# Kernel optimization log

Measured on AMD Instinct MI355X. Metric: run time of the kernel, lower is better.

The kernel has to match this reference:

```python
import math
import jax, jax.numpy as jnp
import numpy as np

B, NQ, NK, DIM, H, HD = 2, 1024, 2048, 1024, 16, 64


def setup_inputs() -> dict:
    key = jax.random.key(0)
    ks = jax.random.split(key, 12)
    s = 1.0 / math.sqrt(DIM)
    return {
        "q": jax.random.normal(ks[0], (B, NQ, DIM), jnp.float32),
        "k": jax.random.normal(ks[1], (B, NK, DIM), jnp.float32),
        "v": jax.random.normal(ks[2], (B, NK, DIM), jnp.float32),
        "distances": jax.random.uniform(ks[3], (B, NQ, NK), jnp.float32),
        "attn_mask": jax.random.bernoulli(ks[4], 0.5, (B, NQ, NK)),
        "key_padding_mask_q": jax.random.bernoulli(ks[5], 0.5, (B, NQ)),
        "key_padding_mask_k": jax.random.bernoulli(ks[6], 0.5, (B, NK)),
        "Wq": jax.random.normal(ks[7], (H * HD, DIM), jnp.float32) * s,
        "Wk": jax.random.normal(ks[8], (H * HD, DIM), jnp.float32) * s,
        "Wv": jax.random.normal(ks[9], (H * HD, DIM), jnp.float32) * s,
        "Wo": jax.random.normal(ks[10], (DIM, H * HD), jnp.float32) * s,
        "gate_alpha": jnp.float32(0.1),
    }


def reference(q, k, v, distances, attn_mask, key_padding_mask_q,
              key_padding_mask_k, Wq, Wk, Wv, Wo, gate_alpha):
    bsz, q_len, _ = q.shape
    k_len = k.shape[1]
    neg = jnp.finfo(q.dtype).min

    # projections -> (B, H, N, HD)
    qp = (q @ Wq.T).reshape(bsz, q_len, H, HD).transpose(0, 2, 1, 3)
    kp = (k @ Wk.T).reshape(bsz, k_len, H, HD).transpose(0, 2, 1, 3)
    vp = (v @ Wv.T).reshape(bsz, k_len, H, HD).transpose(0, 2, 1, 3)

    scores = jnp.einsum('bhqd,bhkd->bhqk', qp, kp) / math.sqrt(HD)
    scores = jnp.where(attn_mask[:, None, :, :], scores, neg)
    scores = jnp.where(key_padding_mask_k[:, None, None, :], scores, neg)

    attn = jax.nn.softmax(scores, axis=-1)  # (B,H,NQ,NK)

    # distance gating: mask, batch-mean normalize, exponential gate
    d = distances * attn_mask.astype(distances.dtype)
    d = d * key_padding_mask_k[:, None, :].astype(d.dtype)
    mean = d.sum(axis=(-1, -2)) / (q_len * k_len + 1e-6)
    mean = jnp.maximum(mean, 1e-6)[:, None, None]
    d = d / mean
    alpha = jax.nn.softplus(gate_alpha)
    gate = jnp.exp(-alpha * d)[:, None, :, :]  # (B,1,NQ,NK)

    w = attn * gate
    w = w / (w.sum(axis=-1, keepdims=True) + 1e-6)

    out = jnp.einsum('bhqk,bhkd->bhqd', w, vp)
    out = out.transpose(0, 2, 1, 3).reshape(bsz, q_len, H * HD)
    out = out * key_padding_mask_q[:, :, None].astype(out.dtype)
    return out @ Wo.T
```

## Files before the change

kernel.cpp:

```cpp
#include <hip/hip_runtime.h>
#include <hip/hip_bf16.h>
#include <cfloat>

#define B_   2
#define NQ_  1024
#define NK_  2048
#define H_   16
#define HD_  64
#define VPAD 2176
#define GPAD 2112
#define NSPLIT 2

typedef float  floatx4 __attribute__((ext_vector_type(4)));
typedef __bf16 bf16x8  __attribute__((ext_vector_type(8)));
typedef __bf16 bf16x4  __attribute__((ext_vector_type(4)));

static __device__ __forceinline__ floatx4 mfma16(bf16x8 a, bf16x8 b, floatx4 c) {
    return __builtin_amdgcn_mfma_f32_16x16x32_bf16(a, b, c, 0, 0, 0);
}

static __device__ __forceinline__ void gl_lds(const __bf16* g, __bf16* lbase,
                                              int lane) {
#if __has_builtin(__builtin_amdgcn_global_load_lds)
    __builtin_amdgcn_global_load_lds(
        (const __attribute__((address_space(1))) void*)g,
        (__attribute__((address_space(3))) void*)lbase, 16, 0, 0);
#else
    *(bf16x8*)(lbase + lane * 8) = *(const bf16x8*)g;
#endif
}

struct CvtArgs {
    const float* src[7];
    __bf16*      dst[7];
};

__global__ __launch_bounds__(256) void cvt_mean_kernel(
    CvtArgs a, const float* __restrict__ dist, const int* __restrict__ amask,
    const int* __restrict__ kpmk, float* __restrict__ msum,
    __bf16* __restrict__ dmask)
{
    if (blockIdx.x >= 7168) {
        const int mb = blockIdx.x - 7168;
        const int b  = mb >> 7;
        const float* d  = dist  + (size_t)b * NQ_ * NK_;
        const int*   am = amask + (size_t)b * NQ_ * NK_;
        const int*   km = kpmk  + b * NK_;
        __bf16*      dm = dmask + (size_t)b * NQ_ * GPAD;
        const int total = NQ_ * NK_ / 4;
        float s = 0.f;
        for (int i = (mb & 127) * 256 + threadIdx.x; i < total; i += 128 * 256) {
            const int idx = i * 4;
            const int kk  = idx & (NK_ - 1);
            const int q   = i >> 9;
            float4 dv = *(const float4*)(d + idx);
            int4   mv = *(const int4*)(am + idx);
            int4   kv = *(const int4*)(km + kk);
            bf16x4 o;
            if (mv.x && kv.x) { s += dv.x; o[0] = (__bf16)dv.x; } else o[0] = (__bf16)3e38f;
            if (mv.y && kv.y) { s += dv.y; o[1] = (__bf16)dv.y; } else o[1] = (__bf16)3e38f;
            if (mv.z && kv.z) { s += dv.z; o[2] = (__bf16)dv.z; } else o[2] = (__bf16)3e38f;
            if (mv.w && kv.w) { s += dv.w; o[3] = (__bf16)dv.w; } else o[3] = (__bf16)3e38f;
            *(bf16x4*)&dm[(size_t)q * GPAD + kk] = o;
        }
        #pragma unroll
        for (int off = 32; off >= 1; off >>= 1) s += __shfl_down(s, off);
        __shared__ float wsum[4];
        if ((threadIdx.x & 63) == 0) wsum[threadIdx.x >> 6] = s;
        __syncthreads();
        if (threadIdx.x == 0)
            atomicAdd(&msum[b], wsum[0] + wsum[1] + wsum[2] + wsum[3]);
        return;
    }
    size_t r = (size_t)blockIdx.x * 256 + threadIdx.x;
    int s;
    if (r < 262144)                  { s = 0; }
    else if ((r -= 262144) < 524288) { s = 1; }
    else if ((r -= 524288) < 524288) { s = 2; }
    else { r -= 524288; s = 3 + (int)(r >> 17); r &= 131071; }
    const float* sp = a.src[s] + r * 8;
    float4 f0 = *(const float4*)sp;
    float4 f1 = *(const float4*)(sp + 4);
    bf16x8 o;
    o[0] = (__bf16)f0.x; o[1] = (__bf16)f0.y; o[2] = (__bf16)f0.z; o[3] = (__bf16)f0.w;
    o[4] = (__bf16)f1.x; o[5] = (__bf16)f1.y; o[6] = (__bf16)f1.z; o[7] = (__bf16)f1.w;
    *(bf16x8*)(a.dst[s] + r * 8) = o;
}

template <typename EPI>
static __device__ __forceinline__ void gemm128_core(
    const __bf16* __restrict__ A, const __bf16* __restrict__ Bw,
    int m0, int n0, __bf16* As, __bf16* Bs, EPI epi)
{
    const int t    = threadIdx.x;
    const int w    = t >> 6, lane = t & 63;
    const int lrow = lane & 15, quad = lane >> 4;
    const int lr   = lane >> 2, lc = lane & 3;

    floatx4 acc[4][4];
    #pragma unroll
    for (int mi = 0; mi < 4; mi++)
        #pragma unroll
        for (int ni = 0; ni < 4; ni++) acc[mi][ni] = floatx4{0.f, 0.f, 0.f, 0.f};

    const __bf16* ga = A  + (size_t)(m0 + w * 32 + lr) * 1024 + lc * 8;
    const __bf16* gb = Bw + (size_t)(n0 + w * 32 + lr) * 1024 + lc * 8;

    for (int k0 = 0; k0 < 1024; k0 += 64) {
        __syncthreads();
        #pragma unroll
        for (int h = 0; h < 2; h++) {
            gl_lds(ga + k0 + h * 32,             &As[h * 4096 + (w * 32) * 32],      lane);
            gl_lds(ga + k0 + h * 32 + 16 * 1024, &As[h * 4096 + (w * 32 + 16) * 32], lane);
            gl_lds(gb + k0 + h * 32,             &Bs[h * 4096 + (w * 32) * 32],      lane);
            gl_lds(gb + k0 + h * 32 + 16 * 1024, &Bs[h * 4096 + (w * 32 + 16) * 32], lane);
        }
        __syncthreads();

        #pragma unroll
        for (int h = 0; h < 2; h++) {
            bf16x8 af[4], bfr[4];
            #pragma unroll
            for (int mi = 0; mi < 4; mi++)
                af[mi] = *(const bf16x8*)
                    &As[h * 4096 + ((w & 1) * 64 + mi * 16 + lrow) * 32 + quad * 8];
            #pragma unroll
            for (int ni = 0; ni < 4; ni++)
                bfr[ni] = *(const bf16x8*)
                    &Bs[h * 4096 + ((w >> 1) * 64 + ni * 16 + lrow) * 32 + quad * 8];
            #pragma unroll
            for (int mi = 0; mi < 4; mi++)
                #pragma unroll
                for (int ni = 0; ni < 4; ni++)
                    acc[mi][ni] = mfma16(af[mi], bfr[ni], acc[mi][ni]);
        }
    }

    #pragma unroll
    for (int mi = 0; mi < 4; mi++)
        #pragma unroll
        for (int ni = 0; ni < 4; ni++)
            #pragma unroll
            for (int r = 0; r < 4; r++) {
                const int m = m0 + (w & 1) * 64 + mi * 16 + quad * 4 + r;
                const int n = n0 + (w >> 1) * 64 + ni * 16 + lrow;
                epi(m, n, acc[mi][ni][r]);
            }
}

template <typename EPI>
static __device__ __forceinline__ void gemm64_core(
    const __bf16* __restrict__ A, const __bf16* __restrict__ Bw,
    int m0, int n0, EPI epi)
{
    __shared__ alignas(16) __bf16 As[2][64 * 32];
    __shared__ alignas(16) __bf16 Bs[2][128 * 32];
    const int t    = threadIdx.x;
    const int w    = t >> 6, lane = t & 63;
    const int lrow = lane & 15, quad = lane >> 4;
    const int lr   = lane >> 2, lc = lane & 3;

    floatx4 acc[4][2];
    #pragma unroll
    for (int mi = 0; mi < 4; mi++)
        #pragma unroll
        for (int ni = 0; ni < 2; ni++) acc[mi][ni] = floatx4{0.f, 0.f, 0.f, 0.f};

    const __bf16* ga = A  + (size_t)(m0 + w * 16 + lr) * 1024 + lc * 8;
    const __bf16* gb = Bw + (size_t)(n0 + w * 32 + lr) * 1024 + lc * 8;

    for (int k0 = 0; k0 < 1024; k0 += 64) {
        __syncthreads();
        #pragma unroll
        for (int h = 0; h < 2; h++) {
            gl_lds(ga + k0 + h * 32,             &As[h][(w * 16) * 32],      lane);
            gl_lds(gb + k0 + h * 32,             &Bs[h][(w * 32) * 32],      lane);
            gl_lds(gb + k0 + h * 32 + 16 * 1024, &Bs[h][(w * 32 + 16) * 32], lane);
        }
        __syncthreads();

        #pragma unroll
        for (int h = 0; h < 2; h++) {
            bf16x8 af[4], bfr[2];
            #pragma unroll
            for (int mi = 0; mi < 4; mi++)
                af[mi] = *(const bf16x8*)
                    &As[h][(mi * 16 + lrow) * 32 + quad * 8];
            #pragma unroll
            for (int ni = 0; ni < 2; ni++)
                bfr[ni] = *(const bf16x8*)
                    &Bs[h][(w * 32 + ni * 16 + lrow) * 32 + quad * 8];
            #pragma unroll
            for (int mi = 0; mi < 4; mi++)
                #pragma unroll
                for (int ni = 0; ni < 2; ni++)
                    acc[mi][ni] = mfma16(af[mi], bfr[ni], acc[mi][ni]);
        }
    }

    #pragma unroll
    for (int mi = 0; mi < 4; mi++)
        #pragma unroll
        for (int ni = 0; ni < 2; ni++)
            #pragma unroll
            for (int r = 0; r < 4; r++) {
                const int m = m0 + mi * 16 + quad * 4 + r;
                const int n = n0 + w * 32 + ni * 16 + lrow;
                epi(m, n, acc[mi][ni][r]);
            }
}

__global__ __launch_bounds__(256) void proj_kernel(
    const __bf16* __restrict__ qb, const __bf16* __restrict__ kb,
    const __bf16* __restrict__ vb, const __bf16* __restrict__ wqb,
    const __bf16* __restrict__ wkb, const __bf16* __restrict__ wvb,
    __bf16* __restrict__ qp, __bf16* __restrict__ kp,
    __bf16* __restrict__ vpT)
{
    __shared__ alignas(16) __bf16 As[2 * 128 * 32];
    __shared__ alignas(16) __bf16 Bs[2 * 128 * 32];
    const int z = blockIdx.z;
    if (z == 0) {
        if ((int)blockIdx.x >= 16) return;
        gemm128_core(qb, wqb, blockIdx.x * 128, blockIdx.y * 128, As, Bs,
                     [&](int m, int n, float v) {
            const int b = m >> 10, q = m & 1023;
            const int h = n >> 6,  d = n & 63;
            qp[(((size_t)(b * 16 + h) * NQ_ + q) << 6) + d] = (__bf16)v;
        });
    } else if (z == 1) {
        gemm128_core(kb, wkb, blockIdx.x * 128, blockIdx.y * 128, As, Bs,
                     [&](int m, int n, float v) {
            const int b = m >> 11, key = m & 2047;
            const int h = n >> 6,  d = n & 63;
            kp[(((size_t)(b * 16 + h) * NK_ + key) << 6) + d] = (__bf16)v;
        });
    } else {
        gemm128_core(wvb, vb, blockIdx.y * 128, blockIdx.x * 128, As, Bs,
                     [&](int m, int n, float v) {
            const int h = m >> 6,  d = m & 63;
            const int b = n >> 11, key = n & 2047;
            vpT[((size_t)(b * 16 + h) * HD_ + d) * VPAD + key] = (__bf16)v;
        });
    }
}

__global__ __launch_bounds__(256) void oproj_kernel(
    const __bf16* __restrict__ A, const __bf16* __restrict__ W,
    float* __restrict__ Cout)
{
    const int m0 = blockIdx.x * 64, n0 = blockIdx.y * 128;
    gemm64_core(A, W, m0, n0, [&](int m, int n, float v) {
        Cout[(size_t)m * 1024 + n] = v;
    });
}

__global__ __launch_bounds__(256, 2) void attn_kernel(
    const __bf16* __restrict__ qp, const __bf16* __restrict__ kp,
    const __bf16* __restrict__ vpT, const __bf16* __restrict__ dmask,
    const float* __restrict__ msum, const float* __restrict__ galpha,
    float* __restrict__ Opart, float* __restrict__ Gpart)
{
    __shared__ __bf16 Ks[64 * 72];
    __shared__ __bf16 Vt[2][64 * 72];
    __shared__ __bf16 Ps[4][2][32 * 72];
    const int t    = threadIdx.x;
    const int w    = t >> 6, lane = t & 63;
    const int lrow = lane & 15, quad = lane >> 4;
    const int qt   = blockIdx.x;
    const int bh   = blockIdx.y;
    const int sp   = blockIdx.z;
    const int b    = bh >> 4;
    const int q0   = qt * 128 + w * 32;
    const int k0   = sp * (NK_ / NSPLIT);
    const int NT   = (NK_ / NSPLIT) / 64;

    const float mean  = fmaxf(msum[b] / ((float)(NQ_ * NK_) + 1e-6f), 1e-6f);
    const float alpha = log1pf(__expf(galpha[0]));
    const float cg    = -alpha / mean;

    bf16x8 qf[2][2];
    #pragma unroll
    for (int qg = 0; qg < 2; qg++) {
        const __bf16* qb = qp + ((size_t)bh * NQ_ + q0 + qg * 16 + lrow) * HD_ +
                           quad * 8;
        qf[qg][0] = *(const bf16x8*)qb;
        qf[qg][1] = *(const bf16x8*)(qb + 32);
    }

    const int srow0 = t >> 3,        sc0 = t & 7;
    const int srow1 = 32 + (t >> 3), sc1 = t & 7;
    const int so0 = srow0 * 72 + sc0 * 8;
    const int so1 = srow1 * 72 + sc1 * 8;
    const __bf16* Kg = kp  + (size_t)bh * NK_ * HD_;
    const __bf16* Vg = vpT + (size_t)bh * HD_ * VPAD;

    const __bf16* grow[2];
    #pragma unroll
    for (int qg = 0; qg < 2; qg++)
        grow[qg] = dmask + ((size_t)b * NQ_ + q0 + qg * 16 + lrow) * GPAD;

    float G[2] = {0.f, 0.f};
    floatx4 O[2][4];
    #pragma unroll
    for (int qg = 0; qg < 2; qg++)
        #pragma unroll
        for (int nb = 0; nb < 4; nb++) O[qg][nb] = floatx4{0.f, 0.f, 0.f, 0.f};

    bf16x8 kr0, kr1, vr0, vr1;
    bf16x4 gr[2][4];
    auto loadt = [&](int kb) {
        kr0 = *(const bf16x8*)(Kg + (size_t)(kb + srow0) * HD_ + sc0 * 8);
        kr1 = *(const bf16x8*)(Kg + (size_t)(kb + srow1) * HD_ + sc1 * 8);
        vr0 = *(const bf16x8*)(Vg + (size_t)srow0 * VPAD + kb + sc0 * 8);
        vr1 = *(const bf16x8*)(Vg + (size_t)srow1 * VPAD + kb + sc1 * 8);
        #pragma unroll
        for (int qg = 0; qg < 2; qg++)
            #pragma unroll
            for (int c = 0; c < 4; c++)
                gr[qg][c] = *(const bf16x4*)(grow[qg] + kb + c * 16 + quad * 4);
    };
    loadt(k0);

    for (int ib = 0; ib < NT; ib++) {
        const int kb  = k0 + ib * 64;
        const int cur = ib & 1;

        __syncthreads();
        *(bf16x8*)&Ks[so0]      = kr0;
        *(bf16x8*)&Ks[so1]      = kr1;
        *(bf16x8*)&Vt[cur][so0] = vr0;
        *(bf16x8*)&Vt[cur][so1] = vr1;
        __syncthreads();

        bf16x4 gcur[2][4];
        #pragma unroll
        for (int qg = 0; qg < 2; qg++)
            #pragma unroll
            for (int c = 0; c < 4; c++) gcur[qg][c] = gr[qg][c];
        if (ib + 1 < NT) loadt(kb + 64);

        bf16x8 kf0[4], kf1[4];
        #pragma unroll
        for (int c = 0; c < 4; c++) {
            kf0[c] = *(const bf16x8*)&Ks[(c * 16 + lrow) * 72 + quad * 8];
            kf1[c] = *(const bf16x8*)&Ks[(c * 16 + lrow) * 72 + 32 + quad * 8];
        }
        floatx4 s4[2][4];
        #pragma unroll
        for (int qg = 0; qg < 2; qg++)
            #pragma unroll
            for (int c = 0; c < 4; c++) {
                floatx4 a = floatx4{0.f, 0.f, 0.f, 0.f};
                a = mfma16(kf0[c], qf[qg][0], a);
                a = mfma16(kf1[c], qf[qg][1], a);
                s4[qg][c] = a;
            }

        if (ib > 0) {
            const int prv = cur ^ 1;
            bf16x8 pf[2][2];
            #pragma unroll
            for (int qg = 0; qg < 2; qg++)
                #pragma unroll
                for (int tt = 0; tt < 2; tt++)
                    pf[qg][tt] = *(const bf16x8*)
                        &Ps[w][prv][(qg * 16 + lrow) * 72 + tt * 32 + quad * 8];
            #pragma unroll
            for (int tt = 0; tt < 2; tt++)
                #pragma unroll
                for (int nb = 0; nb < 4; nb++) {
                    bf16x8 vf = *(const bf16x8*)
                        &Vt[prv][(nb * 16 + lrow) * 72 + tt * 32 + quad * 8];
                    #pragma unroll
                    for (int qg = 0; qg < 2; qg++)
                        O[qg][nb] = mfma16(pf[qg][tt], vf, O[qg][nb]);
                }
        }

        #pragma unroll
        for (int qg = 0; qg < 2; qg++) {
            #pragma unroll
            for (int c = 0; c < 4; c++) {
                const float e0 = __expf(fmaf(s4[qg][c][0], 0.125f, cg * (float)gcur[qg][c][0]));
                const float e1 = __expf(fmaf(s4[qg][c][1], 0.125f, cg * (float)gcur[qg][c][1]));
                const float e2 = __expf(fmaf(s4[qg][c][2], 0.125f, cg * (float)gcur[qg][c][2]));
                const float e3 = __expf(fmaf(s4[qg][c][3], 0.125f, cg * (float)gcur[qg][c][3]));
                G[qg] += (e0 + e1) + (e2 + e3);
                bf16x4 pk;
                pk[0] = (__bf16)e0; pk[1] = (__bf16)e1;
                pk[2] = (__bf16)e2; pk[3] = (__bf16)e3;
                *(bf16x4*)&Ps[w][cur][(qg * 16 + lrow) * 72 + c * 16 + quad * 4] = pk;
            }
        }
    }

    {
        const int prv = (NT - 1) & 1;
        bf16x8 pf[2][2];
        #pragma unroll
        for (int qg = 0; qg < 2; qg++)
            #pragma unroll
            for (int tt = 0; tt < 2; tt++)
                pf[qg][tt] = *(const bf16x8*)
                    &Ps[w][prv][(qg * 16 + lrow) * 72 + tt * 32 + quad * 8];
        #pragma unroll
        for (int tt = 0; tt < 2; tt++)
            #pragma unroll
            for (int nb = 0; nb < 4; nb++) {
                bf16x8 vf = *(const bf16x8*)
                    &Vt[prv][(nb * 16 + lrow) * 72 + tt * 32 + quad * 8];
                #pragma unroll
                for (int qg = 0; qg < 2; qg++)
                    O[qg][nb] = mfma16(pf[qg][tt], vf, O[qg][nb]);
            }
    }

    #pragma unroll
    for (int qg = 0; qg < 2; qg++) {
        G[qg] += __shfl_xor(G[qg], 16);
        G[qg] += __shfl_xor(G[qg], 32);
    }
    float* Ob = Opart + ((size_t)(sp * 32 + bh) * NQ_ + q0) * HD_;
    #pragma unroll
    for (int qg = 0; qg < 2; qg++)
        #pragma unroll
        for (int nb = 0; nb < 4; nb++)
            #pragma unroll
            for (int r = 0; r < 4; r++)
                Ob[(size_t)(qg * 16 + quad * 4 + r) * HD_ + nb * 16 + lrow] =
                    O[qg][nb][r];
    if (quad == 0) {
        #pragma unroll
        for (int qg = 0; qg < 2; qg++)
            Gpart[(size_t)(sp * 32 + bh) * NQ_ + q0 + qg * 16 + lrow] = G[qg];
    }
}

__global__ __launch_bounds__(256) void combine_kernel(
    const float* __restrict__ Opart, const float* __restrict__ Gpart,
    const int* __restrict__ kpmq, __bf16* __restrict__ attnout)
{
    const int t  = blockIdx.x * 256 + threadIdx.x;
    const int d4 = (t & 15) * 4;
    const int q  = (t >> 4) & 1023;
    const int bh = t >> 14;
    const int b  = bh >> 4, h = bh & 15;
    float4 o = float4{0.f, 0.f, 0.f, 0.f};
    float  g = 0.f;
    #pragma unroll
    for (int j = 0; j < NSPLIT; j++) {
        float4 oj = *(const float4*)
            (Opart + ((size_t)(j * 32 + bh) * NQ_ + q) * HD_ + d4);
        o.x += oj.x; o.y += oj.y; o.z += oj.z; o.w += oj.w;
        g += Gpart[(size_t)(j * 32 + bh) * NQ_ + q];
    }
    const float f = kpmq[b * NQ_ + q] ? 1.f / (g + 1e-30f) : 0.f;
    bf16x4 r;
    r[0] = (__bf16)(o.x * f);
    r[1] = (__bf16)(o.y * f);
    r[2] = (__bf16)(o.z * f);
    r[3] = (__bf16)(o.w * f);
    *(bf16x4*)&attnout[((size_t)b * NQ_ + q) * 1024 + h * HD_ + d4] = r;
}

extern "C" void kernel_launch(void* const* d_in, const int* in_sizes, int n_in,
                              void* d_out, int out_size, void* d_ws,
                              size_t ws_size, hipStream_t stream)
{
    const float* q      = (const float*)d_in[0];
    const float* k      = (const float*)d_in[1];
    const float* v      = (const float*)d_in[2];
    const float* dist   = (const float*)d_in[3];
    const int*   amask  = (const int*)d_in[4];
    const int*   kpmq   = (const int*)d_in[5];
    const int*   kpmk   = (const int*)d_in[6];
    const float* Wq     = (const float*)d_in[7];
    const float* Wk     = (const float*)d_in[8];
    const float* Wv     = (const float*)d_in[9];
    const float* Wo     = (const float*)d_in[10];
    const float* galpha = (const float*)d_in[11];

    char* p = (char*)d_ws;
    float*  msum = (float*)p;                 p += 256;
    __bf16* qb   = (__bf16*)p;                p += (size_t)2097152 * 2;
    __bf16* kb   = (__bf16*)p;                p += (size_t)4194304 * 2;
    __bf16* vb   = (__bf16*)p;                p += (size_t)4194304 * 2;
    __bf16* wqb  = (__bf16*)p;                p += (size_t)1048576 * 2;
    __bf16* wkb  = (__bf16*)p;                p += (size_t)1048576 * 2;
    __bf16* wvb  = (__bf16*)p;                p += (size_t)1048576 * 2;
    __bf16* wob  = (__bf16*)p;                p += (size_t)1048576 * 2;
    __bf16* qp   = (__bf16*)p;                p += (size_t)2097152 * 2;
    __bf16* kpb  = (__bf16*)p;                p += (size_t)4194304 * 2;
    __bf16* vpT  = (__bf16*)p;                p += (size_t)32 * 64 * VPAD * 2;
    __bf16* dmask = (__bf16*)p;               p += (size_t)2048 * GPAD * 2;
    __bf16* attnout = (__bf16*)p;             p += (size_t)2097152 * 2;
    float*  Opart   = (float*)p;              p += (size_t)NSPLIT * 2097152 * 4;
    float*  Gpart   = (float*)p;              p += (size_t)NSPLIT * 32768 * 4;

    CvtArgs ca;
    ca.src[0] = q;  ca.src[1] = k;  ca.src[2] = v;
    ca.src[3] = Wq; ca.src[4] = Wk; ca.src[5] = Wv; ca.src[6] = Wo;
    ca.dst[0] = qb;  ca.dst[1] = kb;  ca.dst[2] = vb;
    ca.dst[3] = wqb; ca.dst[4] = wkb; ca.dst[5] = wvb; ca.dst[6] = wob;

    hipMemsetAsync(msum, 0, 256, stream);
    cvt_mean_kernel<<<7424, 256, 0, stream>>>(ca, dist, amask, kpmk, msum,
                                              dmask);
    proj_kernel<<<dim3(32, 8, 3), 256, 0, stream>>>(qb, kb, vb, wqb, wkb, wvb,
                                                    qp, kpb, vpT);
    attn_kernel<<<dim3(8, 32, NSPLIT), 256, 0, stream>>>(qp, kpb, vpT, dmask,
                                                         msum, galpha,
                                                         Opart, Gpart);
    combine_kernel<<<2048, 256, 0, stream>>>(Opart, Gpart, kpmq, attnout);
    oproj_kernel<<<dim3(32, 8), 256, 0, stream>>>(attnout, wob, (float*)d_out);
}
```

Baseline: 258.6 us.

## Drop key split in attention, fuse normalization epilogue, and coarsen conversion blocks

The attention kernel no longer splits the key range across two blocks. Each block now handles 64 queries (16 per wave) over the full key length and writes the normalized, query-masked bf16 output directly, which removes the separate combine kernel and the fp32 partial buffers. The conversion/mean kernel also processes four elements per thread with fewer blocks. In exchange each wave reuses every K/V tile across half as many queries, and the loop runs twice as many serial iterations per block.

```diff
diff --git a/kernel.cpp b/kernel.cpp
--- a/kernel.cpp
+++ b/kernel.cpp
@@ -9,7 +9,6 @@
 #define HD_  64
 #define VPAD 2176
 #define GPAD 2112
-#define NSPLIT 2
 
 typedef float  floatx4 __attribute__((ext_vector_type(4)));
 typedef __bf16 bf16x8  __attribute__((ext_vector_type(8)));
@@ -40,16 +39,18 @@
     const int* __restrict__ kpmk, float* __restrict__ msum,
     __bf16* __restrict__ dmask)
 {
-    if (blockIdx.x >= 7168) {
-        const int mb = blockIdx.x - 7168;
-        const int b  = mb >> 7;
+    if (blockIdx.x >= 1792) {
+        const int mb = blockIdx.x - 1792;
+        const int b  = mb >> 9;
         const float* d  = dist  + (size_t)b * NQ_ * NK_;
         const int*   am = amask + (size_t)b * NQ_ * NK_;
         const int*   km = kpmk  + b * NK_;
         __bf16*      dm = dmask + (size_t)b * NQ_ * GPAD;
-        const int total = NQ_ * NK_ / 4;
+        const int base = (mb & 511) * 256 + threadIdx.x;
         float s = 0.f;
-        for (int i = (mb & 127) * 256 + threadIdx.x; i < total; i += 128 * 256) {
+        #pragma unroll
+        for (int j = 0; j < 4; j++) {
+            const int i   = base + j * 131072;
             const int idx = i * 4;
             const int kk  = idx & (NK_ - 1);
             const int q   = i >> 9;
@@ -72,19 +73,22 @@
             atomicAdd(&msum[b], wsum[0] + wsum[1] + wsum[2] + wsum[3]);
         return;
     }
-    size_t r = (size_t)blockIdx.x * 256 + threadIdx.x;
-    int s;
-    if (r < 262144)                  { s = 0; }
-    else if ((r -= 262144) < 524288) { s = 1; }
-    else if ((r -= 524288) < 524288) { s = 2; }
-    else { r -= 524288; s = 3 + (int)(r >> 17); r &= 131071; }
-    const float* sp = a.src[s] + r * 8;
-    float4 f0 = *(const float4*)sp;
-    float4 f1 = *(const float4*)(sp + 4);
-    bf16x8 o;
-    o[0] = (__bf16)f0.x; o[1] = (__bf16)f0.y; o[2] = (__bf16)f0.z; o[3] = (__bf16)f0.w;
-    o[4] = (__bf16)f1.x; o[5] = (__bf16)f1.y; o[6] = (__bf16)f1.z; o[7] = (__bf16)f1.w;
-    *(bf16x8*)(a.dst[s] + r * 8) = o;
+    #pragma unroll
+    for (int j = 0; j < 4; j++) {
+        size_t r = (size_t)blockIdx.x * 1024 + j * 256 + threadIdx.x;
+        int s;
+        if (r < 262144)                  { s = 0; }
+        else if ((r -= 262144) < 524288) { s = 1; }
+        else if ((r -= 524288) < 524288) { s = 2; }
+        else { r -= 524288; s = 3 + (int)(r >> 17); r &= 131071; }
+        const float* sp = a.src[s] + r * 8;
+        float4 f0 = *(const float4*)sp;
+        float4 f1 = *(const float4*)(sp + 4);
+        bf16x8 o;
+        o[0] = (__bf16)f0.x; o[1] = (__bf16)f0.y; o[2] = (__bf16)f0.z; o[3] = (__bf16)f0.w;
+        o[4] = (__bf16)f1.x; o[5] = (__bf16)f1.y; o[6] = (__bf16)f1.z; o[7] = (__bf16)f1.w;
+        *(bf16x8*)(a.dst[s] + r * 8) = o;
+    }
 }
 
 template <typename EPI>
@@ -259,34 +263,27 @@
     const __bf16* __restrict__ qp, const __bf16* __restrict__ kp,
     const __bf16* __restrict__ vpT, const __bf16* __restrict__ dmask,
     const float* __restrict__ msum, const float* __restrict__ galpha,
-    float* __restrict__ Opart, float* __restrict__ Gpart)
+    const int* __restrict__ kpmq, __bf16* __restrict__ attnout)
 {
     __shared__ __bf16 Ks[64 * 72];
     __shared__ __bf16 Vt[2][64 * 72];
-    __shared__ __bf16 Ps[4][2][32 * 72];
+    __shared__ __bf16 Ps[4][2][16 * 72];
     const int t    = threadIdx.x;
     const int w    = t >> 6, lane = t & 63;
     const int lrow = lane & 15, quad = lane >> 4;
     const int qt   = blockIdx.x;
     const int bh   = blockIdx.y;
-    const int sp   = blockIdx.z;
-    const int b    = bh >> 4;
-    const int q0   = qt * 128 + w * 32;
-    const int k0   = sp * (NK_ / NSPLIT);
-    const int NT   = (NK_ / NSPLIT) / 64;
+    const int b    = bh >> 4, h = bh & 15;
+    const int q0   = qt * 64 + w * 16;
+    const int NT   = NK_ / 64;
 
     const float mean  = fmaxf(msum[b] / ((float)(NQ_ * NK_) + 1e-6f), 1e-6f);
     const float alpha = log1pf(__expf(galpha[0]));
     const float cg    = -alpha / mean;
 
-    bf16x8 qf[2][2];
-    #pragma unroll
-    for (int qg = 0; qg < 2; qg++) {
-        const __bf16* qb = qp + ((size_t)bh * NQ_ + q0 + qg * 16 + lrow) * HD_ +
-                           quad * 8;
-        qf[qg][0] = *(const bf16x8*)qb;
-        qf[qg][1] = *(const bf16x8*)(qb + 32);
-    }
+    const __bf16* qb = qp + ((size_t)bh * NQ_ + q0 + lrow) * HD_ + quad * 8;
+    const bf16x8 qf0 = *(const bf16x8*)qb;
+    const bf16x8 qf1 = *(const bf16x8*)(qb + 32);
 
     const int srow0 = t >> 3,        sc0 = t & 7;
     const int srow1 = 32 + (t >> 3), sc1 = t & 7;
@@ -294,36 +291,28 @@
     const int so1 = srow1 * 72 + sc1 * 8;
     const __bf16* Kg = kp  + (size_t)bh * NK_ * HD_;
     const __bf16* Vg = vpT + (size_t)bh * HD_ * VPAD;
-
-    const __bf16* grow[2];
-    #pragma unroll
-    for (int qg = 0; qg < 2; qg++)
-        grow[qg] = dmask + ((size_t)b * NQ_ + q0 + qg * 16 + lrow) * GPAD;
-
-    float G[2] = {0.f, 0.f};
-    floatx4 O[2][4];
-    #pragma unroll
-    for (int qg = 0; qg < 2; qg++)
-        #pragma unroll
-        for (int nb = 0; nb < 4; nb++) O[qg][nb] = floatx4{0.f, 0.f, 0.f, 0.f};
+    const __bf16* grow = dmask + ((size_t)b * NQ_ + q0 + lrow) * GPAD;
+
+    float G = 0.f;
+    floatx4 O[4];
+    #pragma unroll
+    for (int nb = 0; nb < 4; nb++) O[nb] = floatx4{0.f, 0.f, 0.f, 0.f};
 
     bf16x8 kr0, kr1, vr0, vr1;
-    bf16x4 gr[2][4];
+    bf16x4 gr[4];
     auto loadt = [&](int kb) {
         kr0 = *(const bf16x8*)(Kg + (size_t)(kb + srow0) * HD_ + sc0 * 8);
         kr1 = *(const bf16x8*)(Kg + (size_t)(kb + srow1) * HD_ + sc1 * 8);
         vr0 = *(const bf16x8*)(Vg + (size_t)srow0 * VPAD + kb + sc0 * 8);
         vr1 = *(const bf16x8*)(Vg + (size_t)srow1 * VPAD + kb + sc1 * 8);
         #pragma unroll
-        for (int qg = 0; qg < 2; qg++)
-            #pragma unroll
-            for (int c = 0; c < 4; c++)
-                gr[qg][c] = *(const bf16x4*)(grow[qg] + kb + c * 16 + quad * 4);
+        for (int c = 0; c < 4; c++)
+            gr[c] = *(const bf16x4*)(grow + kb + c * 16 + quad * 4);
     };
-    loadt(k0);
+    loadt(0);
 
     for (int ib = 0; ib < NT; ib++) {
-        const int kb  = k0 + ib * 64;
+        const int kb  = ib * 64;
         const int cur = ib & 1;
 
         __syncthreads();
@@ -333,135 +322,78 @@
         *(bf16x8*)&Vt[cur][so1] = vr1;
         __syncthreads();
 
-        bf16x4 gcur[2][4];
-        #pragma unroll
-        for (int qg = 0; qg < 2; qg++)
-            #pragma unroll
-            for (int c = 0; c < 4; c++) gcur[qg][c] = gr[qg][c];
+        bf16x4 gcur[4];
+        #pragma unroll
+        for (int c = 0; c < 4; c++) gcur[c] = gr[c];
         if (ib + 1 < NT) loadt(kb + 64);
 
-        bf16x8 kf0[4], kf1[4];
+        floatx4 s4[4];
         #pragma unroll
         for (int c = 0; c < 4; c++) {
-            kf0[c] = *(const bf16x8*)&Ks[(c * 16 + lrow) * 72 + quad * 8];
-            kf1[c] = *(const bf16x8*)&Ks[(c * 16 + lrow) * 72 + 32 + quad * 8];
-        }
-        floatx4 s4[2][4];
-        #pragma unroll
-        for (int qg = 0; qg < 2; qg++)
-            #pragma unroll
-            for (int c = 0; c < 4; c++) {
-                floatx4 a = floatx4{0.f, 0.f, 0.f, 0.f};
-                a = mfma16(kf0[c], qf[qg][0], a);
-                a = mfma16(kf1[c], qf[qg][1], a);
-                s4[qg][c] = a;
-            }
+            bf16x8 kf0 = *(const bf16x8*)&Ks[(c * 16 + lrow) * 72 + quad * 8];
+            bf16x8 kf1 = *(const bf16x8*)&Ks[(c * 16 + lrow) * 72 + 32 + quad * 8];
+            floatx4 a = floatx4{0.f, 0.f, 0.f, 0.f};
+            a = mfma16(kf0, qf0, a);
+            a = mfma16(kf1, qf1, a);
+            s4[c] = a;
+        }
 
         if (ib > 0) {
             const int prv = cur ^ 1;
-            bf16x8 pf[2][2];
-            #pragma unroll
-            for (int qg = 0; qg < 2; qg++)
-                #pragma unroll
-                for (int tt = 0; tt < 2; tt++)
-                    pf[qg][tt] = *(const bf16x8*)
-                        &Ps[w][prv][(qg * 16 + lrow) * 72 + tt * 32 + quad * 8];
-            #pragma unroll
-            for (int tt = 0; tt < 2; tt++)
-                #pragma unroll
-                for (int nb = 0; nb < 4; nb++) {
-                    bf16x8 vf = *(const bf16x8*)
-                        &Vt[prv][(nb * 16 + lrow) * 72 + tt * 32 + quad * 8];
-                    #pragma unroll
-                    for (int qg = 0; qg < 2; qg++)
-                        O[qg][nb] = mfma16(pf[qg][tt], vf, O[qg][nb]);
-                }
-        }
-
-        #pragma unroll
-        for (int qg = 0; qg < 2; qg++) {
-            #pragma unroll
-            for (int c = 0; c < 4; c++) {
-                const float e0 = __expf(fmaf(s4[qg][c][0], 0.125f, cg * (float)gcur[qg][c][0]));
-                const float e1 = __expf(fmaf(s4[qg][c][1], 0.125f, cg * (float)gcur[qg][c][1]));
-                const float e2 = __expf(fmaf(s4[qg][c][2], 0.125f, cg * (float)gcur[qg][c][2]));
-                const float e3 = __expf(fmaf(s4[qg][c][3], 0.125f, cg * (float)gcur[qg][c][3]));
-                G[qg] += (e0 + e1) + (e2 + e3);
-                bf16x4 pk;
-                pk[0] = (__bf16)e0; pk[1] = (__bf16)e1;
-                pk[2] = (__bf16)e2; pk[3] = (__bf16)e3;
-                *(bf16x4*)&Ps[w][cur][(qg * 16 + lrow) * 72 + c * 16 + quad * 4] = pk;
+            bf16x8 pf0 = *(const bf16x8*)&Ps[w][prv][lrow * 72 + quad * 8];
+            bf16x8 pf1 = *(const bf16x8*)&Ps[w][prv][lrow * 72 + 32 + quad * 8];
+            #pragma unroll
+            for (int nb = 0; nb < 4; nb++) {
+                bf16x8 vf0 = *(const bf16x8*)
+                    &Vt[prv][(nb * 16 + lrow) * 72 + quad * 8];
+                bf16x8 vf1 = *(const bf16x8*)
+                    &Vt[prv][(nb * 16 + lrow) * 72 + 32 + quad * 8];
+                O[nb] = mfma16(pf0, vf0, O[nb]);
+                O[nb] = mfma16(pf1, vf1, O[nb]);
             }
+        }
+
+        #pragma unroll
+        for (int c = 0; c < 4; c++) {
+            const float e0 = __expf(fmaf(s4[c][0], 0.125f, cg * (float)gcur[c][0]));
+            const float e1 = __expf(fmaf(s4[c][1], 0.125f, cg * (float)gcur[c][1]));
+            const float e2 = __expf(fmaf(s4[c][2], 0.125f, cg * (float)gcur[c][2]));
+            const float e3 = __expf(fmaf(s4[c][3], 0.125f, cg * (float)gcur[c][3]));
+            G += (e0 + e1) + (e2 + e3);
+            bf16x4 pk;
+            pk[0] = (__bf16)e0; pk[1] = (__bf16)e1;
+            pk[2] = (__bf16)e2; pk[3] = (__bf16)e3;
+            *(bf16x4*)&Ps[w][cur][lrow * 72 + c * 16 + quad * 4] = pk;
         }
     }
 
     {
         const int prv = (NT - 1) & 1;
-        bf16x8 pf[2][2];
-        #pragma unroll
-        for (int qg = 0; qg < 2; qg++)
-            #pragma unroll
-            for (int tt = 0; tt < 2; tt++)
-                pf[qg][tt] = *(const bf16x8*)
-                    &Ps[w][prv][(qg * 16 + lrow) * 72 + tt * 32 + quad * 8];
-        #pragma unroll
-        for (int tt = 0; tt < 2; tt++)
-            #pragma unroll
-            for (int nb = 0; nb < 4; nb++) {
-                bf16x8 vf = *(const bf16x8*)
-                    &Vt[prv][(nb * 16 + lrow) * 72 + tt * 32 + quad * 8];
-                #pragma unroll
-                for (int qg = 0; qg < 2; qg++)
-                    O[qg][nb] = mfma16(pf[qg][tt], vf, O[qg][nb]);
-            }
-    }
-
-    #pragma unroll
-    for (int qg = 0; qg < 2; qg++) {
-        G[qg] += __shfl_xor(G[qg], 16);
-        G[qg] += __shfl_xor(G[qg], 32);
-    }
-    float* Ob = Opart + ((size_t)(sp * 32 + bh) * NQ_ + q0) * HD_;
-    #pragma unroll
-    for (int qg = 0; qg < 2; qg++)
-        #pragma unroll
-        for (int nb = 0; nb < 4; nb++)
-            #pragma unroll
-            for (int r = 0; r < 4; r++)
-                Ob[(size_t)(qg * 16 + quad * 4 + r) * HD_ + nb * 16 + lrow] =
-                    O[qg][nb][r];
-    if (quad == 0) {
-        #pragma unroll
-        for (int qg = 0; qg < 2; qg++)
-            Gpart[(size_t)(sp * 32 + bh) * NQ_ + q0 + qg * 16 + lrow] = G[qg];
-    }
-}
-
-__global__ __launch_bounds__(256) void combine_kernel(
-    const float* __restrict__ Opart, const float* __restrict__ Gpart,
-    const int* __restrict__ kpmq, __bf16* __restrict__ attnout)
-{
-    const int t  = blockIdx.x * 256 + threadIdx.x;
-    const int d4 = (t & 15) * 4;
-    const int q  = (t >> 4) & 1023;
-    const int bh = t >> 14;
-    const int b  = bh >> 4, h = bh & 15;
-    float4 o = float4{0.f, 0.f, 0.f, 0.f};
-    float  g = 0.f;
-    #pragma unroll
-    for (int j = 0; j < NSPLIT; j++) {
-        float4 oj = *(const float4*)
-            (Opart + ((size_t)(j * 32 + bh) * NQ_ + q) * HD_ + d4);
-        o.x += oj.x; o.y += oj.y; o.z += oj.z; o.w += oj.w;
-        g += Gpart[(size_t)(j * 32 + bh) * NQ_ + q];
-    }
-    const float f = kpmq[b * NQ_ + q] ? 1.f / (g + 1e-30f) : 0.f;
-    bf16x4 r;
-    r[0] = (__bf16)(o.x * f);
-    r[1] = (__bf16)(o.y * f);
-    r[2] = (__bf16)(o.z * f);
-    r[3] = (__bf16)(o.w * f);
-    *(bf16x4*)&attnout[((size_t)b * NQ_ + q) * 1024 + h * HD_ + d4] = r;
+        bf16x8 pf0 = *(const bf16x8*)&Ps[w][prv][lrow * 72 + quad * 8];
+        bf16x8 pf1 = *(const bf16x8*)&Ps[w][prv][lrow * 72 + 32 + quad * 8];
+        #pragma unroll
+        for (int nb = 0; nb < 4; nb++) {
+            bf16x8 vf0 = *(const bf16x8*)&Vt[prv][(nb * 16 + lrow) * 72 + quad * 8];
+            bf16x8 vf1 = *(const bf16x8*)&Vt[prv][(nb * 16 + lrow) * 72 + 32 + quad * 8];
+            O[nb] = mfma16(pf0, vf0, O[nb]);
+            O[nb] = mfma16(pf1, vf1, O[nb]);
+        }
+    }
+
+    G += __shfl_xor(G, 16);
+    G += __shfl_xor(G, 32);
+
+    #pragma unroll
+    for (int r = 0; r < 4; r++) {
+        const int q  = q0 + quad * 4 + r;
+        const float gq = __shfl(G, quad * 4 + r);
+        const float f  = kpmq[b * NQ_ + q] ? 1.f / (gq + 1e-30f) : 0.f;
+        #pragma unroll
+        for (int nb = 0; nb < 4; nb++) {
+            attnout[((size_t)b * NQ_ + q) * 1024 + h * HD_ + nb * 16 + lrow] =
+                (__bf16)(O[nb][r] * f);
+        }
+    }
 }
 
 extern "C" void kernel_launch(void* const* d_in, const int* in_sizes, int n_in,
@@ -495,8 +427,6 @@
     __bf16* vpT  = (__bf16*)p;                p += (size_t)32 * 64 * VPAD * 2;
     __bf16* dmask = (__bf16*)p;               p += (size_t)2048 * GPAD * 2;
     __bf16* attnout = (__bf16*)p;             p += (size_t)2097152 * 2;
-    float*  Opart   = (float*)p;              p += (size_t)NSPLIT * 2097152 * 4;
-    float*  Gpart   = (float*)p;              p += (size_t)NSPLIT * 32768 * 4;
 
     CvtArgs ca;
     ca.src[0] = q;  ca.src[1] = k;  ca.src[2] = v;
@@ -505,13 +435,11 @@
     ca.dst[3] = wqb; ca.dst[4] = wkb; ca.dst[5] = wvb; ca.dst[6] = wob;
 
     hipMemsetAsync(msum, 0, 256, stream);
-    cvt_mean_kernel<<<7424, 256, 0, stream>>>(ca, dist, amask, kpmk, msum,
+    cvt_mean_kernel<<<2816, 256, 0, stream>>>(ca, dist, amask, kpmk, msum,
                                               dmask);
     proj_kernel<<<dim3(32, 8, 3), 256, 0, stream>>>(qb, kb, vb, wqb, wkb, wvb,
                                                     qp, kpb, vpT);
-    attn_kernel<<<dim3(8, 32, NSPLIT), 256, 0, stream>>>(qp, kpb, vpT, dmask,
-                                                         msum, galpha,
-                                                         Opart, Gpart);
-    combine_kernel<<<2048, 256, 0, stream>>>(Opart, Gpart, kpmq, attnout);
+    attn_kernel<<<dim3(16, 32), 256, 0, stream>>>(qp, kpb, vpT, dmask,
+                                                  msum, galpha, kpmq, attnout);
     oproj_kernel<<<dim3(32, 8), 256, 0, stream>>>(attnout, wob, (float*)d_out);
 }
```

After: 245.6 us. 1.05x faster.
